# Kernel optimization log

Measured on AMD Instinct MI355X. Metric: run time of the kernel, lower is better.

## Reference

```python
import jax, jax.numpy as jnp
import numpy as np

N = 100000
E = 1000000
HID = 64


def gcn_conv(x, W, b, edge_index, edge_w, num_nodes):
    # PyG GCNConv with edge_weight: add self-loops (weight 1), symmetric norm,
    # out[c] = sum_e norm_e * (x @ W)[row_e] aggregated at col_e, plus bias.
    xw = x @ W  # [N, hid]
    row = jnp.concatenate([edge_index[0], jnp.arange(num_nodes)])
    col = jnp.concatenate([edge_index[1], jnp.arange(num_nodes)])
    ew = jnp.concatenate([edge_w, jnp.ones((num_nodes,), x.dtype)])
    deg = jax.ops.segment_sum(ew, col, num_segments=num_nodes)
    dinv = jnp.where(deg > 0, jax.lax.rsqrt(deg), 0.0)
    norm = dinv[row] * ew * dinv[col]  # [E+N]
    msgs = norm[:, None] * xw[row]  # [E+N, hid]
    out = jax.ops.segment_sum(msgs, col, num_segments=num_nodes)
    return out + b


def setup_inputs() -> dict:
    key = jax.random.key(0)
    ks = jax.random.split(key, 12)
    user_x = jax.random.normal(ks[0], (N, 3), jnp.float32)
    movie_x = jax.random.normal(ks[1], (N, 18), jnp.float32)
    edge_index = jax.random.randint(ks[2], (2, E), 0, N, jnp.int64)
    edge_attr = jax.random.uniform(ks[3], (E,), jnp.float32)
    def lin(k, fan_in, fan_out):
        bound = 1.0 / np.sqrt(fan_in)
        k1, k2 = jax.random.split(k)
        W = jax.random.uniform(k1, (fan_in, fan_out), jnp.float32, -bound, bound)
        b = jax.random.uniform(k2, (fan_out,), jnp.float32, -bound, bound)
        return W, b
    W_user, b_user = lin(ks[4], 3, HID)
    W_movie, b_movie = lin(ks[5], 18, HID)
    W1, b1 = lin(ks[6], 2 * HID, 128)
    W2, b2 = lin(ks[7], 128, 1)
    return {"user_x": user_x, "movie_x": movie_x, "edge_index": edge_index,
            "edge_attr": edge_attr, "W_user": W_user, "b_user": b_user,
            "W_movie": W_movie, "b_movie": b_movie, "W1": W1, "b1": b1,
            "W2": W2, "b2": b2}


def reference(user_x, movie_x, edge_index, edge_attr, W_user, b_user,
              W_movie, b_movie, W1, b1, W2, b2):
    user_out = gcn_conv(user_x, W_user, b_user, edge_index, edge_attr, N)
    movie_out = gcn_conv(movie_x, W_movie, b_movie, edge_index, edge_attr, N)
    h = jnp.concatenate([user_out, movie_out], axis=-1)  # [N, 128]
    h = jax.nn.relu(h @ W1 + b1)
    rating_pred = h @ W2 + b2  # [N, 1]
    return rating_pred
```

## Files before the change

### kernel.cpp

```cpp
#include <hip/hip_runtime.h>

#define NN 100000
#define NE 1000000
#define BSH 7
#define BCOLS 128
#define NBUCK 782
#define SBLK 256
#define CAP 2048

__global__ __launch_bounds__(128) void fuse_kernel(const float* __restrict__ Wu,
                                                   const float* __restrict__ bu,
                                                   const float* __restrict__ Wm,
                                                   const float* __restrict__ bm,
                                                   const float* __restrict__ W1,
                                                   const float* __restrict__ b1,
                                                   const float* __restrict__ W2,
                                                   float* __restrict__ Mt,
                                                   int* __restrict__ cnt) {
    const int j = threadIdx.x;
    for (int i = j; i < NBUCK; i += 128) cnt[i] = 0;

    float w1c[128];
#pragma unroll
    for (int k = 0; k < 128; k++) w1c[k] = W1[k * 128 + j];

    float* row = Mt + j * 24;
#pragma unroll
    for (int m = 0; m < 3; m++) {
        float acc = 0.f;
#pragma unroll
        for (int k = 0; k < 64; k++) acc = fmaf(Wu[m * 64 + k], w1c[k], acc);
        row[m] = acc;
    }
#pragma unroll
    for (int m = 0; m < 18; m++) {
        float acc = 0.f;
#pragma unroll
        for (int k = 0; k < 64; k++) acc = fmaf(Wm[m * 64 + k], w1c[64 + k], acc);
        row[3 + m] = acc;
    }
    float bp = b1[j];
#pragma unroll
    for (int k = 0; k < 64; k++) {
        bp = fmaf(bu[k], w1c[k], bp);
        bp = fmaf(bm[k], w1c[64 + k], bp);
    }
    row[21] = bp;
    row[22] = W2[j];
    row[23] = 0.f;
}

__global__ __launch_bounds__(256) void bcnt_kernel(const int* __restrict__ col,
                                                   int* __restrict__ cnt) {
    __shared__ int h[NBUCK];
    for (int i = threadIdx.x; i < NBUCK; i += 256) h[i] = 0;
    __syncthreads();
    for (int e = blockIdx.x * 256 + threadIdx.x; e < NE; e += SBLK * 256)
        atomicAdd(&h[col[e] >> BSH], 1);
    __syncthreads();
    for (int i = threadIdx.x; i < NBUCK; i += 256)
        if (h[i]) atomicAdd(&cnt[i], h[i]);
}

__global__ __launch_bounds__(1024) void bscan_kernel(const int* __restrict__ cnt,
                                                     int* __restrict__ gbase,
                                                     int* __restrict__ H0) {
    __shared__ int s[1024];
    const int t = threadIdx.x;
    const int v = (t < NBUCK) ? cnt[t] : 0;
    s[t] = v;
    __syncthreads();
    for (int off = 1; off < 1024; off <<= 1) {
        int x = (t >= off) ? s[t - off] : 0;
        __syncthreads();
        s[t] += x;
        __syncthreads();
    }
    const int excl = s[t] - v;
    if (t < NBUCK) { gbase[t] = excl; H0[t] = excl; }
    if (t == 0) H0[NBUCK] = NE;
}

__global__ __launch_bounds__(256) void bscatter_kernel(const int* __restrict__ ei,
                                                       const float* __restrict__ ew,
                                                       int* __restrict__ gbase,
                                                       int2* __restrict__ mid) {
    __shared__ int h[NBUCK];
    __shared__ int rbase[NBUCK];
    for (int i = threadIdx.x; i < NBUCK; i += 256) h[i] = 0;
    __syncthreads();
    for (int e = blockIdx.x * 256 + threadIdx.x; e < NE; e += SBLK * 256)
        atomicAdd(&h[ei[NE + e] >> BSH], 1);
    __syncthreads();
    for (int i = threadIdx.x; i < NBUCK; i += 256) {
        const int c0 = h[i];
        rbase[i] = c0 ? atomicAdd(&gbase[i], c0) : 0;
        h[i] = 0;
    }
    __syncthreads();
    for (int e = blockIdx.x * 256 + threadIdx.x; e < NE; e += SBLK * 256) {
        const int c = ei[NE + e];
        const int r = ei[e];
        const float w = ew[e];
        const int b = c >> BSH;
        const int pos = rbase[b] + atomicAdd(&h[b], 1);
        mid[pos] = make_int2((c & (BCOLS - 1)) | (r << BSH), __float_as_int(w));
    }
}

__global__ __launch_bounds__(256) void bdeg_pack_kernel(const int2* __restrict__ mid,
                                                        const int* __restrict__ H0,
                                                        const float* __restrict__ ux,
                                                        const float* __restrict__ mx,
                                                        float* __restrict__ pack) {
    __shared__ float dl[BCOLS];
    const int b = blockIdx.x;
    const int t = threadIdx.x;
    if (t < BCOLS) dl[t] = 0.f;
    __syncthreads();
    const int start = H0[b];
    const int end = H0[b + 1];
    for (int i = start + t; i < end; i += 256) {
        const int2 p = mid[i];
        atomicAdd(&dl[p.x & (BCOLS - 1)], __int_as_float(p.y));
    }
    __syncthreads();
    if (t < BCOLS) {
        const int c = b * BCOLS + t;
        if (c < NN) dl[t] = rsqrtf(dl[t] + 1.0f);
    }
    __syncthreads();
    const size_t obase = (size_t)b * BCOLS * 24;
    for (int f = t; f < BCOLS * 24; f += 256) {
        const int rl = f / 24;
        const int m = f - rl * 24;
        const int r = b * BCOLS + rl;
        if (r < NN) {
            const float d = dl[rl];
            float v;
            if (m < 3) v = d * ux[(size_t)r * 3 + m];
            else if (m < 21) v = d * mx[(size_t)r * 18 + (m - 3)];
            else if (m == 21) v = d;
            else v = 0.f;
            pack[obase + f] = v;
        }
    }
}

__global__ __launch_bounds__(256) void bagg_mlp_kernel(const int2* __restrict__ mid,
                                                       const int* __restrict__ H0,
                                                       const float* __restrict__ pack,
                                                       const float* __restrict__ Mt,
                                                       const float* __restrict__ b2,
                                                       float* __restrict__ out) {
    __shared__ int2 smid[CAP];
    __shared__ int cbase[BCOLS];
    __shared__ int ccur[BCOLS];
    __shared__ float sp[BCOLS][21];
    __shared__ float po[BCOLS];

    const int b = blockIdx.x;
    const int t = threadIdx.x;
    const int col = t & (BCOLS - 1);
    const int hf = t >> 7;
    const int start = H0[b];
    const int end = H0[b + 1];
    const int seg = end - start;
    const int segc = seg < CAP ? seg : CAP;

    if (t < BCOLS) ccur[t] = 0;
    __syncthreads();
    for (int i = t; i < segc; i += 256)
        atomicAdd(&ccur[mid[start + i].x & (BCOLS - 1)], 1);
    __syncthreads();

    int myc = 0;
    if (t < BCOLS) { myc = ccur[t]; cbase[t] = myc; }
    __syncthreads();
    for (int off = 1; off < BCOLS; off <<= 1) {
        int x = 0;
        if (t < BCOLS && t >= off) x = cbase[t - off];
        __syncthreads();
        if (t < BCOLS) cbase[t] += x;
        __syncthreads();
    }
    if (t < BCOLS) ccur[t] = cbase[t] - myc;
    __syncthreads();

    for (int i = t; i < segc; i += 256) {
        const int2 p = mid[start + i];
        const int pos = atomicAdd(&ccur[p.x & (BCOLS - 1)], 1);
        smid[pos] = p;
    }
    __syncthreads();

    float s21[21];
#pragma unroll
    for (int m = 0; m < 21; m++) s21[m] = 0.f;

    const int s0 = (col == 0) ? 0 : cbase[col - 1];
    const int s1 = cbase[col];
#pragma unroll 2
    for (int i = s0 + hf; i < s1; i += 2) {
        const int2 p = smid[i];
        const unsigned row = ((unsigned)p.x) >> BSH;
        const float w = __int_as_float(p.y);
        const float4* pr = (const float4*)(pack + (size_t)row * 24);
        const float4 v0 = pr[0];
        const float4 v1 = pr[1];
        const float4 v2 = pr[2];
        const float4 v3 = pr[3];
        const float4 v4 = pr[4];
        const float4 v5 = pr[5];
        s21[0]  = fmaf(w, v0.x, s21[0]);
        s21[1]  = fmaf(w, v0.y, s21[1]);
        s21[2]  = fmaf(w, v0.z, s21[2]);
        s21[3]  = fmaf(w, v0.w, s21[3]);
        s21[4]  = fmaf(w, v1.x, s21[4]);
        s21[5]  = fmaf(w, v1.y, s21[5]);
        s21[6]  = fmaf(w, v1.z, s21[6]);
        s21[7]  = fmaf(w, v1.w, s21[7]);
        s21[8]  = fmaf(w, v2.x, s21[8]);
        s21[9]  = fmaf(w, v2.y, s21[9]);
        s21[10] = fmaf(w, v2.z, s21[10]);
        s21[11] = fmaf(w, v2.w, s21[11]);
        s21[12] = fmaf(w, v3.x, s21[12]);
        s21[13] = fmaf(w, v3.y, s21[13]);
        s21[14] = fmaf(w, v3.z, s21[14]);
        s21[15] = fmaf(w, v3.w, s21[15]);
        s21[16] = fmaf(w, v4.x, s21[16]);
        s21[17] = fmaf(w, v4.y, s21[17]);
        s21[18] = fmaf(w, v4.z, s21[18]);
        s21[19] = fmaf(w, v4.w, s21[19]);
        s21[20] = fmaf(w, v5.x, s21[20]);
    }

    if (hf) {
#pragma unroll
        for (int m = 0; m < 21; m++) sp[col][m] = s21[m];
    }
    __syncthreads();

    const int c = b * BCOLS + col;
    if (!hf) {
#pragma unroll
        for (int m = 0; m < 21; m++) s21[m] += sp[col][m];
        if (seg > CAP) {
            for (int i = CAP; i < seg; i++) {
                const int2 p = mid[start + i];
                if ((p.x & (BCOLS - 1)) == col) {
                    const unsigned row = ((unsigned)p.x) >> BSH;
                    const float w = __int_as_float(p.y);
                    const float* pr = pack + (size_t)row * 24;
#pragma unroll
                    for (int m = 0; m < 21; m++) s21[m] = fmaf(w, pr[m], s21[m]);
                }
            }
        }
        if (c < NN) {
            const float4* pr = (const float4*)(pack + (size_t)c * 24);
            const float4 v0 = pr[0];
            const float4 v1 = pr[1];
            const float4 v2 = pr[2];
            const float4 v3 = pr[3];
            const float4 v4 = pr[4];
            const float4 v5 = pr[5];
            const float d = v5.y;
            s21[0]  = d * (s21[0]  + v0.x);
            s21[1]  = d * (s21[1]  + v0.y);
            s21[2]  = d * (s21[2]  + v0.z);
            s21[3]  = d * (s21[3]  + v0.w);
            s21[4]  = d * (s21[4]  + v1.x);
            s21[5]  = d * (s21[5]  + v1.y);
            s21[6]  = d * (s21[6]  + v1.z);
            s21[7]  = d * (s21[7]  + v1.w);
            s21[8]  = d * (s21[8]  + v2.x);
            s21[9]  = d * (s21[9]  + v2.y);
            s21[10] = d * (s21[10] + v2.z);
            s21[11] = d * (s21[11] + v2.w);
            s21[12] = d * (s21[12] + v3.x);
            s21[13] = d * (s21[13] + v3.y);
            s21[14] = d * (s21[14] + v3.z);
            s21[15] = d * (s21[15] + v3.w);
            s21[16] = d * (s21[16] + v4.x);
            s21[17] = d * (s21[17] + v4.y);
            s21[18] = d * (s21[18] + v4.z);
            s21[19] = d * (s21[19] + v4.w);
            s21[20] = d * (s21[20] + v5.x);
        }
#pragma unroll
        for (int m = 0; m < 21; m++) sp[col][m] = s21[m];
    }
    __syncthreads();
    if (hf) {
#pragma unroll
        for (int m = 0; m < 21; m++) s21[m] = sp[col][m];
    }

    float o = 0.f;
    const int k0 = hf * 64;
#pragma unroll 4
    for (int k = k0; k < k0 + 64; k++) {
        const float* r = Mt + k * 24;
        float hsum = r[21];
#pragma unroll
        for (int m = 0; m < 21; m++) hsum = fmaf(s21[m], r[m], hsum);
        o = fmaf(fmaxf(hsum, 0.f), r[22], o);
    }
    if (hf) po[col] = o;
    __syncthreads();
    if (!hf && c < NN) out[c] = o + po[col] + b2[0];
}

extern "C" void kernel_launch(void* const* d_in, const int* in_sizes, int n_in,
                              void* d_out, int out_size, void* d_ws, size_t ws_size,
                              hipStream_t stream) {
    const float* ux = (const float*)d_in[0];
    const float* mx = (const float*)d_in[1];
    const int* ei = (const int*)d_in[2];
    const float* ew = (const float*)d_in[3];
    const float* Wu = (const float*)d_in[4];
    const float* bu = (const float*)d_in[5];
    const float* Wm = (const float*)d_in[6];
    const float* bm = (const float*)d_in[7];
    const float* W1 = (const float*)d_in[8];
    const float* b1 = (const float*)d_in[9];
    const float* W2 = (const float*)d_in[10];
    const float* b2 = (const float*)d_in[11];
    float* out = (float*)d_out;

    char* ws = (char*)d_ws;
    int*   cnt   = (int*)ws;
    int*   gbase = (int*)(ws + 4096);
    int*   H0    = (int*)(ws + 8192);
    float* Mt    = (float*)(ws + 12288);
    float* pack  = (float*)(ws + 24576);
    int2*  mid   = (int2*)(ws + 9624576);

    fuse_kernel<<<1, 128, 0, stream>>>(Wu, bu, Wm, bm, W1, b1, W2, Mt, cnt);
    bcnt_kernel<<<SBLK, 256, 0, stream>>>(ei + NE, cnt);
    bscan_kernel<<<1, 1024, 0, stream>>>(cnt, gbase, H0);
    bscatter_kernel<<<SBLK, 256, 0, stream>>>(ei, ew, gbase, mid);
    bdeg_pack_kernel<<<NBUCK, 256, 0, stream>>>(mid, H0, ux, mx, pack);
    bagg_mlp_kernel<<<NBUCK, 256, 0, stream>>>(mid, H0, pack, Mt, b2, out);
}
```

Baseline: 211.9 us.

## Replace bucketed CSR build with per-node counting sort and global-atomic degree

Swaps the 128-column bucket sort plus in-block shared-memory re-sort for a full per-destination-node CSR built with global atomics. Degree is accumulated alongside the counts, and the pack step is fused into the offset scan. The aggregation kernel then assigns four lanes per node and reduces with shuffles, which drops the shared-memory staging and the overflow path. The cost is about 2M contended global atomics for counting and 1M for scatter, plus a nondeterministic edge order within each node.

```diff
diff --git a/kernel.cpp b/kernel.cpp
--- a/kernel.cpp
+++ b/kernel.cpp
@@ -2,24 +2,24 @@
 
 #define NN 100000
 #define NE 1000000
-#define BSH 7
-#define BCOLS 128
-#define NBUCK 782
-#define SBLK 256
-#define CAP 2048
-
-__global__ __launch_bounds__(128) void fuse_kernel(const float* __restrict__ Wu,
-                                                   const float* __restrict__ bu,
-                                                   const float* __restrict__ Wm,
-                                                   const float* __restrict__ bm,
-                                                   const float* __restrict__ W1,
-                                                   const float* __restrict__ b1,
-                                                   const float* __restrict__ W2,
-                                                   float* __restrict__ Mt,
-                                                   int* __restrict__ cnt) {
+#define NBLK 98
+#define CPB 64
+
+__global__ __launch_bounds__(128) void fuse_zero_kernel(const float* __restrict__ Wu,
+                                                        const float* __restrict__ bu,
+                                                        const float* __restrict__ Wm,
+                                                        const float* __restrict__ bm,
+                                                        const float* __restrict__ W1,
+                                                        const float* __restrict__ b1,
+                                                        const float* __restrict__ W2,
+                                                        float* __restrict__ Mt,
+                                                        int* __restrict__ zbuf) {
+    if (blockIdx.x != 0) {
+        for (int i = (blockIdx.x - 1) * 128 + threadIdx.x; i < 2 * NN; i += 256 * 128)
+            zbuf[i] = 0;
+        return;
+    }
     const int j = threadIdx.x;
-    for (int i = j; i < NBUCK; i += 128) cnt[i] = 0;
-
     float w1c[128];
 #pragma unroll
     for (int k = 0; k < 128; k++) w1c[k] = W1[k * 128 + j];
@@ -50,24 +50,60 @@
     row[23] = 0.f;
 }
 
-__global__ __launch_bounds__(256) void bcnt_kernel(const int* __restrict__ col,
-                                                   int* __restrict__ cnt) {
-    __shared__ int h[NBUCK];
-    for (int i = threadIdx.x; i < NBUCK; i += 256) h[i] = 0;
+__global__ __launch_bounds__(256) void cnt_deg_kernel(const int* __restrict__ ei,
+                                                      const float* __restrict__ ew,
+                                                      int* __restrict__ cnt,
+                                                      float* __restrict__ degf) {
+    for (int e = blockIdx.x * 256 + threadIdx.x; e < NE; e += 1024 * 256) {
+        const int c = ei[NE + e];
+        atomicAdd(&cnt[c], 1);
+        atomicAdd(&degf[c], ew[e]);
+    }
+}
+
+__global__ __launch_bounds__(1024) void bsum_kernel(const int* __restrict__ cnt,
+                                                    int* __restrict__ bsum) {
+    __shared__ int s[1024];
+    const int g = blockIdx.x * 1024 + threadIdx.x;
+    s[threadIdx.x] = (g < NN) ? cnt[g] : 0;
     __syncthreads();
-    for (int e = blockIdx.x * 256 + threadIdx.x; e < NE; e += SBLK * 256)
-        atomicAdd(&h[col[e] >> BSH], 1);
+    for (int off = 512; off > 0; off >>= 1) {
+        if (threadIdx.x < off) s[threadIdx.x] += s[threadIdx.x + off];
+        __syncthreads();
+    }
+    if (threadIdx.x == 0) bsum[blockIdx.x] = s[0];
+}
+
+__global__ __launch_bounds__(128) void bscan_kernel(const int* __restrict__ bsum,
+                                                    int* __restrict__ bbase,
+                                                    int* __restrict__ H0) {
+    __shared__ int s[128];
+    const int t = threadIdx.x;
+    const int v = (t < NBLK) ? bsum[t] : 0;
+    s[t] = v;
     __syncthreads();
-    for (int i = threadIdx.x; i < NBUCK; i += 256)
-        if (h[i]) atomicAdd(&cnt[i], h[i]);
-}
-
-__global__ __launch_bounds__(1024) void bscan_kernel(const int* __restrict__ cnt,
-                                                     int* __restrict__ gbase,
-                                                     int* __restrict__ H0) {
+    for (int off = 1; off < 128; off <<= 1) {
+        int x = (t >= off) ? s[t - off] : 0;
+        __syncthreads();
+        s[t] += x;
+        __syncthreads();
+    }
+    if (t < NBLK) bbase[t] = s[t] - v;
+    if (t == 0) H0[NN] = NE;
+}
+
+__global__ __launch_bounds__(1024) void offs_pack_kernel(const int* __restrict__ cnt,
+                                                         const float* __restrict__ degf,
+                                                         const int* __restrict__ bbase,
+                                                         int* __restrict__ H0,
+                                                         int* __restrict__ cur,
+                                                         const float* __restrict__ ux,
+                                                         const float* __restrict__ mx,
+                                                         float* __restrict__ pack) {
     __shared__ int s[1024];
     const int t = threadIdx.x;
-    const int v = (t < NBUCK) ? cnt[t] : 0;
+    const int g = blockIdx.x * 1024 + t;
+    const int v = (g < NN) ? cnt[g] : 0;
     s[t] = v;
     __syncthreads();
     for (int off = 1; off < 1024; off <<= 1) {
@@ -76,74 +112,35 @@
         s[t] += x;
         __syncthreads();
     }
-    const int excl = s[t] - v;
-    if (t < NBUCK) { gbase[t] = excl; H0[t] = excl; }
-    if (t == 0) H0[NBUCK] = NE;
-}
-
-__global__ __launch_bounds__(256) void bscatter_kernel(const int* __restrict__ ei,
-                                                       const float* __restrict__ ew,
-                                                       int* __restrict__ gbase,
-                                                       int2* __restrict__ mid) {
-    __shared__ int h[NBUCK];
-    __shared__ int rbase[NBUCK];
-    for (int i = threadIdx.x; i < NBUCK; i += 256) h[i] = 0;
-    __syncthreads();
-    for (int e = blockIdx.x * 256 + threadIdx.x; e < NE; e += SBLK * 256)
-        atomicAdd(&h[ei[NE + e] >> BSH], 1);
-    __syncthreads();
-    for (int i = threadIdx.x; i < NBUCK; i += 256) {
-        const int c0 = h[i];
-        rbase[i] = c0 ? atomicAdd(&gbase[i], c0) : 0;
-        h[i] = 0;
-    }
-    __syncthreads();
-    for (int e = blockIdx.x * 256 + threadIdx.x; e < NE; e += SBLK * 256) {
+    if (g < NN) {
+        const int base = bbase[blockIdx.x] + s[t] - v;
+        H0[g] = base;
+        cur[g] = base;
+        const float d = rsqrtf(degf[g] + 1.0f);
+        float* pr = pack + (size_t)g * 24;
+        const float* u = ux + (size_t)g * 3;
+        const float* m = mx + (size_t)g * 18;
+        pr[0] = d * u[0];
+        pr[1] = d * u[1];
+        pr[2] = d * u[2];
+#pragma unroll
+        for (int k = 0; k < 18; k++) pr[3 + k] = d * m[k];
+        pr[21] = d;
+        pr[22] = 0.f;
+        pr[23] = 0.f;
+    }
+}
+
+__global__ __launch_bounds__(256) void scatter_kernel(const int* __restrict__ ei,
+                                                      const float* __restrict__ ew,
+                                                      int* __restrict__ cur,
+                                                      int2* __restrict__ mid) {
+    for (int e = blockIdx.x * 256 + threadIdx.x; e < NE; e += 1024 * 256) {
         const int c = ei[NE + e];
         const int r = ei[e];
         const float w = ew[e];
-        const int b = c >> BSH;
-        const int pos = rbase[b] + atomicAdd(&h[b], 1);
-        mid[pos] = make_int2((c & (BCOLS - 1)) | (r << BSH), __float_as_int(w));
-    }
-}
-
-__global__ __launch_bounds__(256) void bdeg_pack_kernel(const int2* __restrict__ mid,
-                                                        const int* __restrict__ H0,
-                                                        const float* __restrict__ ux,
-                                                        const float* __restrict__ mx,
-                                                        float* __restrict__ pack) {
-    __shared__ float dl[BCOLS];
-    const int b = blockIdx.x;
-    const int t = threadIdx.x;
-    if (t < BCOLS) dl[t] = 0.f;
-    __syncthreads();
-    const int start = H0[b];
-    const int end = H0[b + 1];
-    for (int i = start + t; i < end; i += 256) {
-        const int2 p = mid[i];
-        atomicAdd(&dl[p.x & (BCOLS - 1)], __int_as_float(p.y));
-    }
-    __syncthreads();
-    if (t < BCOLS) {
-        const int c = b * BCOLS + t;
-        if (c < NN) dl[t] = rsqrtf(dl[t] + 1.0f);
-    }
-    __syncthreads();
-    const size_t obase = (size_t)b * BCOLS * 24;
-    for (int f = t; f < BCOLS * 24; f += 256) {
-        const int rl = f / 24;
-        const int m = f - rl * 24;
-        const int r = b * BCOLS + rl;
-        if (r < NN) {
-            const float d = dl[rl];
-            float v;
-            if (m < 3) v = d * ux[(size_t)r * 3 + m];
-            else if (m < 21) v = d * mx[(size_t)r * 18 + (m - 3)];
-            else if (m == 21) v = d;
-            else v = 0.f;
-            pack[obase + f] = v;
-        }
+        const int pos = atomicAdd(&cur[c], 1);
+        mid[pos] = make_int2(r, __float_as_int(w));
     }
 }
 
@@ -153,163 +150,102 @@
                                                        const float* __restrict__ Mt,
                                                        const float* __restrict__ b2,
                                                        float* __restrict__ out) {
-    __shared__ int2 smid[CAP];
-    __shared__ int cbase[BCOLS];
-    __shared__ int ccur[BCOLS];
-    __shared__ float sp[BCOLS][21];
-    __shared__ float po[BCOLS];
-
-    const int b = blockIdx.x;
     const int t = threadIdx.x;
-    const int col = t & (BCOLS - 1);
-    const int hf = t >> 7;
-    const int start = H0[b];
-    const int end = H0[b + 1];
-    const int seg = end - start;
-    const int segc = seg < CAP ? seg : CAP;
-
-    if (t < BCOLS) ccur[t] = 0;
-    __syncthreads();
-    for (int i = t; i < segc; i += 256)
-        atomicAdd(&ccur[mid[start + i].x & (BCOLS - 1)], 1);
-    __syncthreads();
-
-    int myc = 0;
-    if (t < BCOLS) { myc = ccur[t]; cbase[t] = myc; }
-    __syncthreads();
-    for (int off = 1; off < BCOLS; off <<= 1) {
-        int x = 0;
-        if (t < BCOLS && t >= off) x = cbase[t - off];
-        __syncthreads();
-        if (t < BCOLS) cbase[t] += x;
-        __syncthreads();
-    }
-    if (t < BCOLS) ccur[t] = cbase[t] - myc;
-    __syncthreads();
-
-    for (int i = t; i < segc; i += 256) {
-        const int2 p = mid[start + i];
-        const int pos = atomicAdd(&ccur[p.x & (BCOLS - 1)], 1);
-        smid[pos] = p;
-    }
-    __syncthreads();
+    const int sub = t & 3;
+    const int c = blockIdx.x * CPB + (t >> 2);
 
     float s21[21];
 #pragma unroll
     for (int m = 0; m < 21; m++) s21[m] = 0.f;
 
-    const int s0 = (col == 0) ? 0 : cbase[col - 1];
-    const int s1 = cbase[col];
-#pragma unroll 2
-    for (int i = s0 + hf; i < s1; i += 2) {
-        const int2 p = smid[i];
-        const unsigned row = ((unsigned)p.x) >> BSH;
-        const float w = __int_as_float(p.y);
-        const float4* pr = (const float4*)(pack + (size_t)row * 24);
+    if (c < NN) {
+        const int s0 = H0[c];
+        const int s1 = H0[c + 1];
+        for (int i = s0 + sub; i < s1; i += 4) {
+            const int2 p = mid[i];
+            const float w = __int_as_float(p.y);
+            const float4* pr = (const float4*)(pack + (size_t)p.x * 24);
+            const float4 v0 = pr[0];
+            const float4 v1 = pr[1];
+            const float4 v2 = pr[2];
+            const float4 v3 = pr[3];
+            const float4 v4 = pr[4];
+            const float4 v5 = pr[5];
+            s21[0]  = fmaf(w, v0.x, s21[0]);
+            s21[1]  = fmaf(w, v0.y, s21[1]);
+            s21[2]  = fmaf(w, v0.z, s21[2]);
+            s21[3]  = fmaf(w, v0.w, s21[3]);
+            s21[4]  = fmaf(w, v1.x, s21[4]);
+            s21[5]  = fmaf(w, v1.y, s21[5]);
+            s21[6]  = fmaf(w, v1.z, s21[6]);
+            s21[7]  = fmaf(w, v1.w, s21[7]);
+            s21[8]  = fmaf(w, v2.x, s21[8]);
+            s21[9]  = fmaf(w, v2.y, s21[9]);
+            s21[10] = fmaf(w, v2.z, s21[10]);
+            s21[11] = fmaf(w, v2.w, s21[11]);
+            s21[12] = fmaf(w, v3.x, s21[12]);
+            s21[13] = fmaf(w, v3.y, s21[13]);
+            s21[14] = fmaf(w, v3.z, s21[14]);
+            s21[15] = fmaf(w, v3.w, s21[15]);
+            s21[16] = fmaf(w, v4.x, s21[16]);
+            s21[17] = fmaf(w, v4.y, s21[17]);
+            s21[18] = fmaf(w, v4.z, s21[18]);
+            s21[19] = fmaf(w, v4.w, s21[19]);
+            s21[20] = fmaf(w, v5.x, s21[20]);
+        }
+    }
+
+#pragma unroll
+    for (int m = 0; m < 21; m++) {
+        s21[m] += __shfl_xor(s21[m], 1);
+        s21[m] += __shfl_xor(s21[m], 2);
+    }
+
+    float o = 0.f;
+    if (c < NN) {
+        const float4* pr = (const float4*)(pack + (size_t)c * 24);
         const float4 v0 = pr[0];
         const float4 v1 = pr[1];
         const float4 v2 = pr[2];
         const float4 v3 = pr[3];
         const float4 v4 = pr[4];
         const float4 v5 = pr[5];
-        s21[0]  = fmaf(w, v0.x, s21[0]);
-        s21[1]  = fmaf(w, v0.y, s21[1]);
-        s21[2]  = fmaf(w, v0.z, s21[2]);
-        s21[3]  = fmaf(w, v0.w, s21[3]);
-        s21[4]  = fmaf(w, v1.x, s21[4]);
-        s21[5]  = fmaf(w, v1.y, s21[5]);
-        s21[6]  = fmaf(w, v1.z, s21[6]);
-        s21[7]  = fmaf(w, v1.w, s21[7]);
-        s21[8]  = fmaf(w, v2.x, s21[8]);
-        s21[9]  = fmaf(w, v2.y, s21[9]);
-        s21[10] = fmaf(w, v2.z, s21[10]);
-        s21[11] = fmaf(w, v2.w, s21[11]);
-        s21[12] = fmaf(w, v3.x, s21[12]);
-        s21[13] = fmaf(w, v3.y, s21[13]);
-        s21[14] = fmaf(w, v3.z, s21[14]);
-        s21[15] = fmaf(w, v3.w, s21[15]);
-        s21[16] = fmaf(w, v4.x, s21[16]);
-        s21[17] = fmaf(w, v4.y, s21[17]);
-        s21[18] = fmaf(w, v4.z, s21[18]);
-        s21[19] = fmaf(w, v4.w, s21[19]);
-        s21[20] = fmaf(w, v5.x, s21[20]);
-    }
-
-    if (hf) {
-#pragma unroll
-        for (int m = 0; m < 21; m++) sp[col][m] = s21[m];
-    }
-    __syncthreads();
-
-    const int c = b * BCOLS + col;
-    if (!hf) {
-#pragma unroll
-        for (int m = 0; m < 21; m++) s21[m] += sp[col][m];
-        if (seg > CAP) {
-            for (int i = CAP; i < seg; i++) {
-                const int2 p = mid[start + i];
-                if ((p.x & (BCOLS - 1)) == col) {
-                    const unsigned row = ((unsigned)p.x) >> BSH;
-                    const float w = __int_as_float(p.y);
-                    const float* pr = pack + (size_t)row * 24;
-#pragma unroll
-                    for (int m = 0; m < 21; m++) s21[m] = fmaf(w, pr[m], s21[m]);
-                }
-            }
+        const float d = v5.y;
+        s21[0]  = d * (s21[0]  + v0.x);
+        s21[1]  = d * (s21[1]  + v0.y);
+        s21[2]  = d * (s21[2]  + v0.z);
+        s21[3]  = d * (s21[3]  + v0.w);
+        s21[4]  = d * (s21[4]  + v1.x);
+        s21[5]  = d * (s21[5]  + v1.y);
+        s21[6]  = d * (s21[6]  + v1.z);
+        s21[7]  = d * (s21[7]  + v1.w);
+        s21[8]  = d * (s21[8]  + v2.x);
+        s21[9]  = d * (s21[9]  + v2.y);
+        s21[10] = d * (s21[10] + v2.z);
+        s21[11] = d * (s21[11] + v2.w);
+        s21[12] = d * (s21[12] + v3.x);
+        s21[13] = d * (s21[13] + v3.y);
+        s21[14] = d * (s21[14] + v3.z);
+        s21[15] = d * (s21[15] + v3.w);
+        s21[16] = d * (s21[16] + v4.x);
+        s21[17] = d * (s21[17] + v4.y);
+        s21[18] = d * (s21[18] + v4.z);
+        s21[19] = d * (s21[19] + v4.w);
+        s21[20] = d * (s21[20] + v5.x);
+
+        const int k0 = sub * 32;
+#pragma unroll 2
+        for (int k = k0; k < k0 + 32; k++) {
+            const float* r = Mt + k * 24;
+            float h = r[21];
+#pragma unroll
+            for (int m = 0; m < 21; m++) h = fmaf(s21[m], r[m], h);
+            o = fmaf(fmaxf(h, 0.f), r[22], o);
         }
-        if (c < NN) {
-            const float4* pr = (const float4*)(pack + (size_t)c * 24);
-            const float4 v0 = pr[0];
-            const float4 v1 = pr[1];
-            const float4 v2 = pr[2];
-            const float4 v3 = pr[3];
-            const float4 v4 = pr[4];
-            const float4 v5 = pr[5];
-            const float d = v5.y;
-            s21[0]  = d * (s21[0]  + v0.x);
-            s21[1]  = d * (s21[1]  + v0.y);
-            s21[2]  = d * (s21[2]  + v0.z);
-            s21[3]  = d * (s21[3]  + v0.w);
-            s21[4]  = d * (s21[4]  + v1.x);
-            s21[5]  = d * (s21[5]  + v1.y);
-            s21[6]  = d * (s21[6]  + v1.z);
-            s21[7]  = d * (s21[7]  + v1.w);
-            s21[8]  = d * (s21[8]  + v2.x);
-            s21[9]  = d * (s21[9]  + v2.y);
-            s21[10] = d * (s21[10] + v2.z);
-            s21[11] = d * (s21[11] + v2.w);
-            s21[12] = d * (s21[12] + v3.x);
-            s21[13] = d * (s21[13] + v3.y);
-            s21[14] = d * (s21[14] + v3.z);
-            s21[15] = d * (s21[15] + v3.w);
-            s21[16] = d * (s21[16] + v4.x);
-            s21[17] = d * (s21[17] + v4.y);
-            s21[18] = d * (s21[18] + v4.z);
-            s21[19] = d * (s21[19] + v4.w);
-            s21[20] = d * (s21[20] + v5.x);
-        }
-#pragma unroll
-        for (int m = 0; m < 21; m++) sp[col][m] = s21[m];
-    }
-    __syncthreads();
-    if (hf) {
-#pragma unroll
-        for (int m = 0; m < 21; m++) s21[m] = sp[col][m];
-    }
-
-    float o = 0.f;
-    const int k0 = hf * 64;
-#pragma unroll 4
-    for (int k = k0; k < k0 + 64; k++) {
-        const float* r = Mt + k * 24;
-        float hsum = r[21];
-#pragma unroll
-        for (int m = 0; m < 21; m++) hsum = fmaf(s21[m], r[m], hsum);
-        o = fmaf(fmaxf(hsum, 0.f), r[22], o);
-    }
-    if (hf) po[col] = o;
-    __syncthreads();
-    if (!hf && c < NN) out[c] = o + po[col] + b2[0];
+    }
+    o += __shfl_xor(o, 1);
+    o += __shfl_xor(o, 2);
+    if (sub == 0 && c < NN) out[c] = o + b2[0];
 }
 
 extern "C" void kernel_launch(void* const* d_in, const int* in_sizes, int n_in,
@@ -331,16 +267,20 @@
 
     char* ws = (char*)d_ws;
     int*   cnt   = (int*)ws;
-    int*   gbase = (int*)(ws + 4096);
-    int*   H0    = (int*)(ws + 8192);
-    float* Mt    = (float*)(ws + 12288);
-    float* pack  = (float*)(ws + 24576);
-    int2*  mid   = (int2*)(ws + 9624576);
-
-    fuse_kernel<<<1, 128, 0, stream>>>(Wu, bu, Wm, bm, W1, b1, W2, Mt, cnt);
-    bcnt_kernel<<<SBLK, 256, 0, stream>>>(ei + NE, cnt);
-    bscan_kernel<<<1, 1024, 0, stream>>>(cnt, gbase, H0);
-    bscatter_kernel<<<SBLK, 256, 0, stream>>>(ei, ew, gbase, mid);
-    bdeg_pack_kernel<<<NBUCK, 256, 0, stream>>>(mid, H0, ux, mx, pack);
-    bagg_mlp_kernel<<<NBUCK, 256, 0, stream>>>(mid, H0, pack, Mt, b2, out);
-}
+    float* degf  = (float*)(ws + 400000);
+    int*   cur   = (int*)(ws + 800000);
+    int*   H0    = (int*)(ws + 1200000);
+    int*   bsum  = (int*)(ws + 1600016);
+    int*   bbase = (int*)(ws + 1600416);
+    float* Mt    = (float*)(ws + 1600816);
+    float* pack  = (float*)(ws + 1613104);
+    int2*  mid   = (int2*)(ws + 11213104);
+
+    fuse_zero_kernel<<<257, 128, 0, stream>>>(Wu, bu, Wm, bm, W1, b1, W2, Mt, cnt);
+    cnt_deg_kernel<<<1024, 256, 0, stream>>>(ei, ew, cnt, degf);
+    bsum_kernel<<<NBLK, 1024, 0, stream>>>(cnt, bsum);
+    bscan_kernel<<<1, 128, 0, stream>>>(bsum, bbase, H0);
+    offs_pack_kernel<<<NBLK, 1024, 0, stream>>>(cnt, degf, bbase, H0, cur, ux, mx, pack);
+    scatter_kernel<<<1024, 256, 0, stream>>>(ei, ew, cur, mid);
+    bagg_mlp_kernel<<<(NN + CPB - 1) / CPB, 256, 0, stream>>>(mid, H0, pack, Mt, b2, out);
+}
```

Measured after the change: 434.8 us. 105% more time.
